# Optimization experiments

Measured on AMD Instinct MI355X. Metric: run time of the kernel, lower is better.

The kernel has to match this reference:

```python
import jax, jax.numpy as jnp
import numpy as np

B, HH, WW, C = 16, 56, 56, 384
HEADS, WS, SHIFT, HID = 12, 7, 3, 1536
N = WS * WS
EPS = 1e-5


def _rel_pos_index(ws):
    coords = np.stack(np.meshgrid(np.arange(ws), np.arange(ws), indexing='ij'))  # (2, ws, ws)
    cf = coords.reshape(2, -1)
    rel = (cf[:, :, None] - cf[:, None, :]).transpose(1, 2, 0).copy()  # (N, N, 2)
    rel[:, :, 0] += ws - 1
    rel[:, :, 1] += ws - 1
    rel[:, :, 0] *= 2 * ws - 1
    return rel.sum(-1)  # (N, N) int


def _attn_mask(H, W, ws, shift):
    img = np.zeros((H, W))
    sl = (slice(0, -ws), slice(-ws, -shift), slice(-shift, None))
    cnt = 0
    for h in sl:
        for w in sl:
            img[h, w] = cnt
            cnt += 1
    mw = img.reshape(H // ws, ws, W // ws, ws).transpose(0, 2, 1, 3).reshape(-1, ws * ws)  # (nW, N)
    am = mw[:, None, :] - mw[:, :, None]
    return np.where(am != 0, -100.0, 0.0).astype(np.float32)  # (nW, N, N)

REL_IDX = jnp.asarray(_rel_pos_index(WS))
ATTN_MASK = jnp.asarray(_attn_mask(HH, WW, WS, SHIFT))


def _ln(x, w, b):
    m = x.mean(-1, keepdims=True)
    v = ((x - m) ** 2).mean(-1, keepdims=True)
    return (x - m) * jax.lax.rsqrt(v + EPS) * w + b


def _win_part(x, ws):
    b, h, w, c = x.shape
    x = x.reshape(b, h // ws, ws, w // ws, ws, c).transpose(0, 1, 3, 2, 4, 5)
    return x.reshape(-1, ws * ws, c)


def _win_rev(wins, ws, h, w):
    c = wins.shape[-1]
    b = wins.shape[0] // ((h // ws) * (w // ws))
    x = wins.reshape(b, h // ws, w // ws, ws, ws, c).transpose(0, 1, 3, 2, 4, 5)
    return x.reshape(b, h, w, c)


def setup_inputs() -> dict:
    key = jax.random.key(0)
    ks = jax.random.split(key, 12)
    s = lambda fan: 1.0 / np.sqrt(fan)
    return {
        'x': jax.random.normal(ks[0], (B, HH * WW, C), jnp.float32),
        'norm1_w': jnp.ones((C,), jnp.float32),
        'norm1_b': jnp.zeros((C,), jnp.float32),
        'qkv_w': jax.random.normal(ks[1], (3 * C, C), jnp.float32) * s(C),
        'qkv_b': jnp.zeros((3 * C,), jnp.float32),
        'bias_table': jax.random.normal(ks[2], ((2 * WS - 1) ** 2, HEADS), jnp.float32) * 0.02,
        'proj_w': jax.random.normal(ks[3], (C, C), jnp.float32) * s(C),
        'proj_b': jnp.zeros((C,), jnp.float32),
        'norm2_w': jnp.ones((C,), jnp.float32),
        'norm2_b': jnp.zeros((C,), jnp.float32),
        'mlp_w1': jax.random.normal(ks[4], (HID, C), jnp.float32) * s(C),
        'mlp_b1': jnp.zeros((HID,), jnp.float32),
        'mlp_w2': jax.random.normal(ks[5], (C, HID), jnp.float32) * s(HID),
        'mlp_b2': jnp.zeros((C,), jnp.float32),
        'H': HH,
        'W': WW,
    }


def reference(x, norm1_w, norm1_b, qkv_w, qkv_b, bias_table, proj_w, proj_b,
              norm2_w, norm2_b, mlp_w1, mlp_b1, mlp_w2, mlp_b2, H, W):
    b = x.shape[0]
    shortcut = x
    h = _ln(x, norm1_w, norm1_b).reshape(b, H, W, C)
    # cyclic shift (H, W divisible by WS -> no padding needed)
    h = jnp.roll(h, shift=(-SHIFT, -SHIFT), axis=(1, 2))
    xw = _win_part(h, WS)  # (b*nW, N, C)
    Bw = xw.shape[0]
    hd = C // HEADS
    qkv = xw @ qkv_w.T + qkv_b  # (Bw, N, 3C)
    qkv = qkv.reshape(Bw, N, 3, HEADS, hd).transpose(2, 0, 3, 1, 4)
    q, k, v = qkv[0], qkv[1], qkv[2]  # (Bw, heads, N, hd)
    attn = jnp.einsum('bhnd,bhmd->bhnm', q * (hd ** -0.5), k)
    rel_bias = bias_table[REL_IDX.reshape(-1)].reshape(N, N, HEADS).transpose(2, 0, 1)
    attn = attn + rel_bias[None]
    nW = ATTN_MASK.shape[0]
    attn = attn.reshape(Bw // nW, nW, HEADS, N, N) + ATTN_MASK[None, :, None]
    attn = jax.nn.softmax(attn.reshape(Bw, HEADS, N, N), axis=-1)
    out = jnp.einsum('bhnm,bhmd->bhnd', attn, v).transpose(0, 2, 1, 3).reshape(Bw, N, C)
    out = out @ proj_w.T + proj_b
    h = _win_rev(out, WS, H, W)
    h = jnp.roll(h, shift=(SHIFT, SHIFT), axis=(1, 2)).reshape(b, H * W, C)
    x = shortcut + h
    y = _ln(x, norm2_w, norm2_b)
    y = jax.nn.gelu(y @ mlp_w1.T + mlp_b1, approximate=False) @ mlp_w2.T + mlp_b2
    return x + y
```

## Files before the change

### kernel.cpp

```cpp
#include <hip/hip_runtime.h>

typedef unsigned short ushort_t;
typedef __attribute__((ext_vector_type(8))) short bf16x8;
typedef __attribute__((ext_vector_type(4))) float f32x4;

__device__ __forceinline__ float b2f(ushort_t u) {
    union { float f; unsigned int u32; } x; x.u32 = ((unsigned int)u) << 16; return x.f;
}
__device__ __forceinline__ ushort_t f2b(float f) {
    union { float f; unsigned int u; } x; x.f = f;
    unsigned int r = x.u + 0x7fffu + ((x.u >> 16) & 1u);
    return (ushort_t)(r >> 16);
}
__device__ __forceinline__ float ldin(const void* p, size_t i, int fp32) {
    return fp32 ? ((const float*)p)[i] : b2f(((const ushort_t*)p)[i]);
}
__device__ __forceinline__ void gl_lds16(const ushort_t* g, ushort_t* l) {
    __builtin_amdgcn_global_load_lds((const __attribute__((address_space(1))) unsigned int*)g,
                                     (__attribute__((address_space(3))) unsigned int*)l, 16, 0, 0);
}
__device__ __forceinline__ float gelu_f(float x) {
    float xx = x * x;
    float u  = x * (0.7978845608028654f + 0.0356774081363f * xx);
    float a  = __builtin_fabsf(u);
    float e2 = __expf(-2.0f * a);
    float t  = (1.0f - e2) * __builtin_amdgcn_rcpf(1.0f + e2);
    t = __builtin_copysignf(t, u);
    return 0.5f * x * (1.0f + t);
}

struct Cv { const void* s; ushort_t* d; int n; };
struct CvA { Cv a[13]; };
__global__ void convert_all(CvA c, int total) {
    int fp32 = (*(const unsigned int*)c.a[0].s == 0x3F800000u);
    for (int idx = blockIdx.x * blockDim.x + threadIdx.x; idx < total; idx += gridDim.x * blockDim.x) {
        int i = idx, k = 0;
        while (k < 12 && i >= c.a[k].n) { i -= c.a[k].n; ++k; }
        c.a[k].d[i] = fp32 ? f2b(((const float*)c.a[k].s)[i]) : ((const ushort_t*)c.a[k].s)[i];
    }
}

__global__ __launch_bounds__(256) void ln_kernel(const void* __restrict__ x,
                                                 const ushort_t* __restrict__ w,
                                                 const ushort_t* __restrict__ bvec,
                                                 ushort_t* __restrict__ out, int mode, int row_base,
                                                 const void* __restrict__ flagsrc)
{
    int wave = threadIdx.x >> 6, lane = threadIdx.x & 63;
    int lr = blockIdx.x * 4 + wave;
    int r = row_base + lr;
    int f32 = (mode == 1) ? 1 : (*(const unsigned int*)flagsrc == 0x3F800000u);
    long src;
    if (mode == 0) {
        int win = r / 49, pos = r % 49;
        int b = win >> 6, wy = (win >> 3) & 7, wx = win & 7;
        int py = pos / 7, px = pos - py * 7;
        int ys = wy * 7 + py + 3; if (ys >= 56) ys -= 56;
        int xs = wx * 7 + px + 3; if (xs >= 56) xs -= 56;
        src = (long)b * 3136 + ys * 56 + xs;
    } else {
        src = r;
    }
    float v[6];
    float s = 0.f, sq = 0.f;
#pragma unroll
    for (int j = 0; j < 6; ++j) {
        v[j] = ldin(x, src * 384 + lane + 64 * j, f32);
        s += v[j]; sq += v[j] * v[j];
    }
#pragma unroll
    for (int off = 32; off; off >>= 1) { s += __shfl_xor(s, off); sq += __shfl_xor(sq, off); }
    float mean = s * (1.f / 384.f);
    float var  = sq * (1.f / 384.f) - mean * mean;
    float rstd = rsqrtf(var + 1e-5f);
    ushort_t* op = out + (size_t)lr * 384;
#pragma unroll
    for (int j = 0; j < 6; ++j) {
        int c = lane + 64 * j;
        op[c] = f2b((v[j] - mean) * rstd * b2f(w[c]) + b2f(bvec[c]));
    }
}

__global__ __launch_bounds__(256) void attn_mfma(const ushort_t* __restrict__ qkv,
                                                 const ushort_t* __restrict__ bt,
                                                 ushort_t* __restrict__ out)
{
    __shared__ __align__(16) ushort_t Pb[4][64 * 72];
    __shared__ __align__(16) ushort_t Vb[4][32 * 72];
    int win = blockIdx.x;
    int t = threadIdx.x;
    int wave = t >> 6, lane = t & 63;
    int quad = lane >> 4, l16 = lane & 15;
    ushort_t* P  = Pb[wave];
    ushort_t* VT = Vb[wave];
    int wimg = win & 63;
    int wy = wimg >> 3, wx = wimg & 7;
    const float scale = 0.17677669529663687f;

    int rjv[4], cjv[4], gjv[4], cvalid[4];
#pragma unroll
    for (int jt = 0; jt < 4; ++jt) {
        int c = jt * 16 + l16;
        cvalid[jt] = (c < 49);
        int rj = c / 7, cj = c - rj * 7;
        rjv[jt] = rj; cjv[jt] = cj;
        int gjy = (wy == 7) ? (rj < 4 ? 1 : 2) : 0;
        int gjx = (wx == 7) ? (cj < 4 ? 1 : 2) : 0;
        gjv[jt] = gjy * 3 + gjx;
    }

    for (int hh = 0; hh < 3; ++hh) {
        int head = wave * 3 + hh;
        size_t base = (size_t)win * 49 * 1152 + (size_t)head * 32;

        bf16x8 qf[4], kf[4];
#pragma unroll
        for (int i = 0; i < 4; ++i) {
            int row = i * 16 + l16;
            bf16x8 z = {};
            qf[i] = z; kf[i] = z;
            if (row < 49) {
                qf[i] = *(const bf16x8*)(qkv + base + (size_t)row * 1152 + quad * 8);
                kf[i] = *(const bf16x8*)(qkv + base + (size_t)row * 1152 + 384 + quad * 8);
            }
        }
#pragma unroll
        for (int e = 0; e < 4; ++e) {
            int j = e * 16 + (lane >> 2);
            int db = (lane & 3) * 8;
            ushort_t buf[8] = {};
            if (j < 49) *(uint4*)buf = *(const uint4*)(qkv + base + (size_t)j * 1152 + 768 + db);
#pragma unroll
            for (int s = 0; s < 8; ++s) VT[(db + s) * 72 + j] = buf[s];
        }

        f32x4 Sv[4][4];
#pragma unroll
        for (int i = 0; i < 4; ++i)
#pragma unroll
            for (int j = 0; j < 4; ++j) {
                f32x4 z = {};
                Sv[i][j] = __builtin_amdgcn_mfma_f32_16x16x32_bf16(qf[i], kf[j], z, 0, 0, 0);
            }

#pragma unroll
        for (int it = 0; it < 4; ++it) {
#pragma unroll
            for (int r = 0; r < 4; ++r) {
                int m = it * 16 + quad * 4 + r;
                int ri = m / 7, ci = m - ri * 7;
                int giy = (wy == 7) ? (ri < 4 ? 1 : 2) : 0;
                int gix = (wx == 7) ? (ci < 4 ? 1 : 2) : 0;
                int gi = giy * 3 + gix;
                float vals[4];
                float vmax = -1e30f;
#pragma unroll
                for (int jt = 0; jt < 4; ++jt) {
                    float sv = -1e30f;
                    if (m < 49 && cvalid[jt]) {
                        int rel = (ri - rjv[jt] + 6) * 13 + (ci - cjv[jt] + 6);
                        sv = Sv[it][jt][r] * scale + b2f(bt[rel * 12 + head]);
                        if (gi != gjv[jt]) sv -= 100.f;
                    }
                    vals[jt] = sv;
                    vmax = fmaxf(vmax, sv);
                }
#pragma unroll
                for (int off = 1; off < 16; off <<= 1) vmax = fmaxf(vmax, __shfl_xor(vmax, off));
                float ssum = 0.f;
#pragma unroll
                for (int jt = 0; jt < 4; ++jt) { float e = __expf(vals[jt] - vmax); vals[jt] = e; ssum += e; }
#pragma unroll
                for (int off = 1; off < 16; off <<= 1) ssum += __shfl_xor(ssum, off);
                float inv = __builtin_amdgcn_rcpf(ssum);
#pragma unroll
                for (int jt = 0; jt < 4; ++jt) P[m * 72 + jt * 16 + l16] = f2b(vals[jt] * inv);
            }
        }

        f32x4 Ov[4][2] = {};
#pragma unroll
        for (int kk = 0; kk < 2; ++kk) {
            bf16x8 vb[2];
            vb[0] = *(const bf16x8*)&VT[(l16) * 72 + kk * 32 + quad * 8];
            vb[1] = *(const bf16x8*)&VT[(16 + l16) * 72 + kk * 32 + quad * 8];
#pragma unroll
            for (int mt = 0; mt < 4; ++mt) {
                bf16x8 pa = *(const bf16x8*)&P[(mt * 16 + l16) * 72 + kk * 32 + quad * 8];
                Ov[mt][0] = __builtin_amdgcn_mfma_f32_16x16x32_bf16(pa, vb[0], Ov[mt][0], 0, 0, 0);
                Ov[mt][1] = __builtin_amdgcn_mfma_f32_16x16x32_bf16(pa, vb[1], Ov[mt][1], 0, 0, 0);
            }
        }
#pragma unroll
        for (int mt = 0; mt < 4; ++mt)
#pragma unroll
            for (int r = 0; r < 4; ++r) {
                int m = mt * 16 + quad * 4 + r;
                if (m < 49) {
                    size_t orow = ((size_t)win * 49 + m) * 384 + (size_t)head * 32;
                    out[orow + l16]      = f2b(Ov[mt][0][r]);
                    out[orow + 16 + l16] = f2b(Ov[mt][1][r]);
                }
            }
    }
}

template <int EPI>
__global__ __launch_bounds__(256) void gemm_k(const ushort_t* __restrict__ A,
                                              const ushort_t* __restrict__ Bw,
                                              const ushort_t* __restrict__ bias,
                                              const void* __restrict__ residv,
                                              void* __restrict__ outv,
                                              int N, int K, long rbase,
                                              const void* __restrict__ flagsrc)
{
    __shared__ __align__(16) ushort_t lA[3][128 * 32];
    __shared__ __align__(16) ushort_t lB[3][128 * 32];

    unsigned gx = gridDim.x;
    unsigned nwg = gx * gridDim.y;
    unsigned lid = blockIdx.y * gx + blockIdx.x;
    unsigned xcd = lid & 7u, chunk_i = lid >> 3;
    unsigned q = nwg >> 3, r8 = nwg & 7u;
    unsigned logical = (xcd < r8 ? xcd * (q + 1) : r8 * (q + 1) + (xcd - r8) * q) + chunk_i;
    int m0 = (int)(logical / gx) * 128, n0 = (int)(logical % gx) * 128;

    int t = threadIdx.x;
    int wave = t >> 6, lane = t & 63;
    int quad = lane >> 4, l16 = lane & 15;
    int wrow = (wave >> 1) * 64, wcol = (wave & 1) * 64;
    f32x4 acc[4][4] = {};

    float bb[4];
#pragma unroll
    for (int j = 0; j < 4; ++j) bb[j] = b2f(bias[n0 + wcol + j * 16 + l16]);
    asm volatile("" :: "v"(bb[0]), "v"(bb[1]), "v"(bb[2]), "v"(bb[3]));

    int srow = wave * 32 + (lane >> 2);
    int fsw  = (srow >> 1) & 3;
    int scol = (((lane & 3) ^ fsw)) * 8;
    const ushort_t* gA0 = A  + (size_t)(m0 + srow) * K + scol;
    const ushort_t* gA1 = gA0 + (size_t)16 * K;
    const ushort_t* gB0 = Bw + (size_t)(n0 + srow) * K + scol;
    const ushort_t* gB1 = gB0 + (size_t)16 * K;

    auto stage = [&](int buf, int k0) {
        gl_lds16(gA0 + k0, &lA[buf][wave * 1024]);
        gl_lds16(gA1 + k0, &lA[buf][wave * 1024 + 512]);
        gl_lds16(gB0 + k0, &lB[buf][wave * 1024]);
        gl_lds16(gB1 + k0, &lB[buf][wave * 1024 + 512]);
    };

    int sl = (quad ^ ((l16 >> 1) & 3)) * 8;
    auto compute = [&](int buf) {
        bf16x8 af[4], bf[4];
#pragma unroll
        for (int i = 0; i < 4; ++i)
            af[i] = *(const bf16x8*)(&lA[buf][(wrow + i * 16 + l16) * 32 + sl]);
#pragma unroll
        for (int j = 0; j < 4; ++j)
            bf[j] = *(const bf16x8*)(&lB[buf][(wcol + j * 16 + l16) * 32 + sl]);
#pragma unroll
        for (int i = 0; i < 4; ++i)
#pragma unroll
            for (int j = 0; j < 4; ++j)
                acc[i][j] = __builtin_amdgcn_mfma_f32_16x16x32_bf16(af[i], bf[j], acc[i][j], 0, 0, 0);
    };

    int T = K >> 5;
    stage(0, 0);
    if (T > 1) stage(1, 32);

    int cur = 0;
    for (int tt = 0; tt < T - 1; ++tt) {
        asm volatile("s_waitcnt vmcnt(4)" ::: "memory");
        __builtin_amdgcn_s_barrier();
        if (tt + 2 < T) stage(cur == 0 ? 2 : cur - 1, (tt + 2) * 32);
        compute(cur);
        cur = (cur == 2) ? 0 : cur + 1;
    }
    asm volatile("s_waitcnt vmcnt(0)" ::: "memory");
    __builtin_amdgcn_s_barrier();
    compute(cur);

    int rf32 = (EPI == 2) ? (*(const unsigned int*)flagsrc == 0x3F800000u) : 1;

#pragma unroll
    for (int i = 0; i < 4; ++i) {
#pragma unroll
        for (int rix = 0; rix < 4; ++rix) {
            int m = m0 + wrow + i * 16 + quad * 4 + rix;
            unsigned orow = 0;
            if (EPI == 2) {
                int mg = (int)rbase + m;
                int win = mg / 49, pos = mg - win * 49;
                int b = win >> 6, wy = (win >> 3) & 7, wx = win & 7;
                int py = pos / 7, px = pos - py * 7;
                int y = wy * 7 + py + 3; if (y >= 56) y -= 56;
                int x = wx * 7 + px + 3; if (x >= 56) x -= 56;
                orow = (unsigned)(b * 3136 + y * 56 + x);
            } else if (EPI == 3) {
                orow = (unsigned)(rbase + m);
            }
#pragma unroll
            for (int j = 0; j < 4; ++j) {
                int n = n0 + wcol + j * 16 + l16;
                float vv = acc[i][j][rix] + bb[j];
                if (EPI == 0) {
                    ((ushort_t*)outv)[(unsigned)m * (unsigned)N + (unsigned)n] = f2b(vv);
                } else if (EPI == 1) {
                    ((ushort_t*)outv)[(unsigned)m * (unsigned)N + (unsigned)n] = f2b(gelu_f(vv));
                } else {
                    float r = ldin(residv, (size_t)orow * 384 + n, rf32);
                    ((float*)outv)[(size_t)orow * 384 + n] = vv + r;
                }
            }
        }
    }
}

extern "C" void kernel_launch(void* const* d_in, const int* in_sizes, int n_in,
                              void* d_out, int out_size, void* d_ws, size_t ws_size,
                              hipStream_t stream)
{
    (void)in_sizes; (void)n_in; (void)out_size;
    char* ws = (char*)d_ws;
    size_t off = 0;
    auto alloc = [&](size_t bytes) { size_t p = off; off = (off + bytes + 255) & ~(size_t)255; return p; };

    size_t o_n1w  = alloc(384 * 2);
    size_t o_n1b  = alloc(384 * 2);
    size_t o_qw   = alloc(442368ull * 2);
    size_t o_qb   = alloc(1152 * 2);
    size_t o_bt   = alloc(2028 * 2);
    size_t o_pw   = alloc(147456ull * 2);
    size_t o_pb   = alloc(384 * 2);
    size_t o_n2w  = alloc(384 * 2);
    size_t o_n2b  = alloc(384 * 2);
    size_t o_w1   = alloc(589824ull * 2);
    size_t o_b1   = alloc(1536 * 2);
    size_t o_w2   = alloc(589824ull * 2);
    size_t o_b2   = alloc(384 * 2);

    size_t avail = (ws_size > off) ? ws_size - off : 0;
    int M_c;
    if      (avail >= (size_t)50176 * 3840 + 1024) M_c = 50176;
    else if (avail >= (size_t)12544 * 3840 + 1024) M_c = 12544;
    else                                            M_c = 6272;
    int nch = 50176 / M_c;
    size_t o_s1 = alloc((size_t)M_c * 768);
    size_t o_s2 = alloc((size_t)M_c * 3072);

    ushort_t* n1w  = (ushort_t*)(ws + o_n1w);
    ushort_t* n1b  = (ushort_t*)(ws + o_n1b);
    ushort_t* qw   = (ushort_t*)(ws + o_qw);
    ushort_t* qb   = (ushort_t*)(ws + o_qb);
    ushort_t* bt   = (ushort_t*)(ws + o_bt);
    ushort_t* pw   = (ushort_t*)(ws + o_pw);
    ushort_t* pb   = (ushort_t*)(ws + o_pb);
    ushort_t* n2w  = (ushort_t*)(ws + o_n2w);
    ushort_t* n2b  = (ushort_t*)(ws + o_n2b);
    ushort_t* w1   = (ushort_t*)(ws + o_w1);
    ushort_t* b1   = (ushort_t*)(ws + o_b1);
    ushort_t* w2   = (ushort_t*)(ws + o_w2);
    ushort_t* b2v  = (ushort_t*)(ws + o_b2);
    ushort_t* s1   = (ushort_t*)(ws + o_s1);
    ushort_t* s2   = (ushort_t*)(ws + o_s2);
    const void* x  = d_in[0];
    const void* fs = d_in[1];
    float* xmid    = (float*)d_out;

    CvA ca;
    ca.a[0]  = {d_in[1],  n1w, 384};
    ca.a[1]  = {d_in[2],  n1b, 384};
    ca.a[2]  = {d_in[3],  qw,  442368};
    ca.a[3]  = {d_in[4],  qb,  1152};
    ca.a[4]  = {d_in[5],  bt,  2028};
    ca.a[5]  = {d_in[6],  pw,  147456};
    ca.a[6]  = {d_in[7],  pb,  384};
    ca.a[7]  = {d_in[8],  n2w, 384};
    ca.a[8]  = {d_in[9],  n2b, 384};
    ca.a[9]  = {d_in[10], w1,  589824};
    ca.a[10] = {d_in[11], b1,  1536};
    ca.a[11] = {d_in[12], w2,  589824};
    ca.a[12] = {d_in[13], b2v, 384};
    convert_all<<<2048, 256, 0, stream>>>(ca, 1776492);

    for (int c = 0; c < nch; ++c) {
        int rb = c * M_c;
        ln_kernel<<<dim3(M_c / 4), dim3(256), 0, stream>>>(x, n1w, n1b, s1, 0, rb, fs);
        gemm_k<0><<<dim3(9, M_c / 128), dim3(256), 0, stream>>>(s1, qw, qb, nullptr, s2, 1152, 384, 0, fs);
        attn_mfma<<<dim3(M_c / 49), dim3(256), 0, stream>>>(s2, bt, s1);
        gemm_k<2><<<dim3(3, M_c / 128), dim3(256), 0, stream>>>(s1, pw, pb, x, xmid, 384, 384, rb, fs);
    }
    for (int c = 0; c < nch; ++c) {
        int rb = c * M_c;
        ln_kernel<<<dim3(M_c / 4), dim3(256), 0, stream>>>(xmid, n2w, n2b, s1, 1, rb, fs);
        gemm_k<1><<<dim3(12, M_c / 128), dim3(256), 0, stream>>>(s1, w1, b1, nullptr, s2, 1536, 384, 0, fs);
        gemm_k<3><<<dim3(3, M_c / 128), dim3(256), 0, stream>>>(s2, w2, b2v, xmid, (float*)d_out, 384, 1536, rb, fs);
    }
}
```

Before: 623.8 us.

## Enlarge GEMM tile to 256x128 with 8 waves per block

Changes the GEMM kernel from 128x128 tiles with 4 waves to 256x128 tiles with 8 waves. Each block now stages 256 A rows and 128 B rows per k-step using three async global-to-LDS loads per wave, with M clamping and bounds checks for a partial last tile. The intent is to reuse each B tile across more rows and cut per-block overhead. In exchange, each block uses more LDS, the grid has fewer blocks (which can hurt occupancy and wave balance), and the prefetch wait count is adjusted.

```diff
diff --git a/kernel.cpp b/kernel.cpp
--- a/kernel.cpp
+++ b/kernel.cpp
@@ -206,15 +206,15 @@
 }
 
 template <int EPI>
-__global__ __launch_bounds__(256) void gemm_k(const ushort_t* __restrict__ A,
-                                              const ushort_t* __restrict__ Bw,
-                                              const ushort_t* __restrict__ bias,
-                                              const void* __restrict__ residv,
-                                              void* __restrict__ outv,
-                                              int N, int K, long rbase,
-                                              const void* __restrict__ flagsrc)
+__global__ __launch_bounds__(512, 4) void gemm_k(const ushort_t* __restrict__ A,
+                                                 const ushort_t* __restrict__ Bw,
+                                                 const ushort_t* __restrict__ bias,
+                                                 const void* __restrict__ residv,
+                                                 void* __restrict__ outv,
+                                                 int N, int K, int Mp, long rbase,
+                                                 const void* __restrict__ flagsrc)
 {
-    __shared__ __align__(16) ushort_t lA[3][128 * 32];
+    __shared__ __align__(16) ushort_t lA[3][256 * 32];
     __shared__ __align__(16) ushort_t lB[3][128 * 32];
 
     unsigned gx = gridDim.x;
@@ -223,7 +223,7 @@
     unsigned xcd = lid & 7u, chunk_i = lid >> 3;
     unsigned q = nwg >> 3, r8 = nwg & 7u;
     unsigned logical = (xcd < r8 ? xcd * (q + 1) : r8 * (q + 1) + (xcd - r8) * q) + chunk_i;
-    int m0 = (int)(logical / gx) * 128, n0 = (int)(logical % gx) * 128;
+    int m0 = (int)(logical / gx) * 256, n0 = (int)(logical % gx) * 128;
 
     int t = threadIdx.x;
     int wave = t >> 6, lane = t & 63;
@@ -236,19 +236,27 @@
     for (int j = 0; j < 4; ++j) bb[j] = b2f(bias[n0 + wcol + j * 16 + l16]);
     asm volatile("" :: "v"(bb[0]), "v"(bb[1]), "v"(bb[2]), "v"(bb[3]));
 
-    int srow = wave * 32 + (lane >> 2);
-    int fsw  = (srow >> 1) & 3;
-    int scol = (((lane & 3) ^ fsw)) * 8;
-    const ushort_t* gA0 = A  + (size_t)(m0 + srow) * K + scol;
-    const ushort_t* gA1 = gA0 + (size_t)16 * K;
-    const ushort_t* gB0 = Bw + (size_t)(n0 + srow) * K + scol;
-    const ushort_t* gB1 = gB0 + (size_t)16 * K;
+    const ushort_t* gp[3];
+    ushort_t* lp[3];
+    int lstr[3];
+#pragma unroll
+    for (int e = 0; e < 3; ++e) {
+        int chunk = wave * 3 + e;
+        int a = (chunk < 16);
+        int trow = (a ? chunk * 16 : (chunk - 16) * 16) + (lane >> 2);
+        int fsw = (trow >> 1) & 3;
+        int scol = ((lane & 3) ^ fsw) * 8;
+        int grow = a ? (m0 + trow) : (n0 + trow);
+        if (a && grow >= Mp) grow = Mp - 1;
+        gp[e] = (a ? A : Bw) + (size_t)grow * K + scol;
+        lp[e] = a ? &lA[0][chunk * 512] : &lB[0][(chunk - 16) * 512];
+        lstr[e] = a ? 256 * 32 : 128 * 32;
+    }
 
     auto stage = [&](int buf, int k0) {
-        gl_lds16(gA0 + k0, &lA[buf][wave * 1024]);
-        gl_lds16(gA1 + k0, &lA[buf][wave * 1024 + 512]);
-        gl_lds16(gB0 + k0, &lB[buf][wave * 1024]);
-        gl_lds16(gB1 + k0, &lB[buf][wave * 1024 + 512]);
+#pragma unroll
+        for (int e = 0; e < 3; ++e)
+            gl_lds16(gp[e] + k0, lp[e] + buf * lstr[e]);
     };
 
     int sl = (quad ^ ((l16 >> 1) & 3)) * 8;
@@ -269,11 +277,11 @@
 
     int T = K >> 5;
     stage(0, 0);
-    if (T > 1) stage(1, 32);
+    stage(1, 32);
 
     int cur = 0;
     for (int tt = 0; tt < T - 1; ++tt) {
-        asm volatile("s_waitcnt vmcnt(4)" ::: "memory");
+        asm volatile("s_waitcnt vmcnt(3)" ::: "memory");
         __builtin_amdgcn_s_barrier();
         if (tt + 2 < T) stage(cur == 0 ? 2 : cur - 1, (tt + 2) * 32);
         compute(cur);
@@ -290,6 +298,7 @@
 #pragma unroll
         for (int rix = 0; rix < 4; ++rix) {
             int m = m0 + wrow + i * 16 + quad * 4 + rix;
+            if (m >= Mp) continue;
             unsigned orow = 0;
             if (EPI == 2) {
                 int mg = (int)rbase + m;
@@ -388,15 +397,17 @@
 
     for (int c = 0; c < nch; ++c) {
         int rb = c * M_c;
+        int gy = (M_c + 255) / 256;
         ln_kernel<<<dim3(M_c / 4), dim3(256), 0, stream>>>(x, n1w, n1b, s1, 0, rb, fs);
-        gemm_k<0><<<dim3(9, M_c / 128), dim3(256), 0, stream>>>(s1, qw, qb, nullptr, s2, 1152, 384, 0, fs);
+        gemm_k<0><<<dim3(9, gy), dim3(512), 0, stream>>>(s1, qw, qb, nullptr, s2, 1152, 384, M_c, 0, fs);
         attn_mfma<<<dim3(M_c / 49), dim3(256), 0, stream>>>(s2, bt, s1);
-        gemm_k<2><<<dim3(3, M_c / 128), dim3(256), 0, stream>>>(s1, pw, pb, x, xmid, 384, 384, rb, fs);
+        gemm_k<2><<<dim3(3, gy), dim3(512), 0, stream>>>(s1, pw, pb, x, xmid, 384, 384, M_c, rb, fs);
     }
     for (int c = 0; c < nch; ++c) {
         int rb = c * M_c;
+        int gy = (M_c + 255) / 256;
         ln_kernel<<<dim3(M_c / 4), dim3(256), 0, stream>>>(xmid, n2w, n2b, s1, 1, rb, fs);
-        gemm_k<1><<<dim3(12, M_c / 128), dim3(256), 0, stream>>>(s1, w1, b1, nullptr, s2, 1536, 384, 0, fs);
-        gemm_k<3><<<dim3(3, M_c / 128), dim3(256), 0, stream>>>(s2, w2, b2v, xmid, (float*)d_out, 384, 1536, rb, fs);
-    }
-}
+        gemm_k<1><<<dim3(12, gy), dim3(512), 0, stream>>>(s1, w1, b1, nullptr, s2, 1536, 384, M_c, 0, fs);
+        gemm_k<3><<<dim3(3, gy), dim3(512), 0, stream>>>(s2, w2, b2v, xmid, (float*)d_out, 384, 1536, M_c, rb, fs);
+    }
+}
```

After: 594.0 us. 1.05x faster.

## Load GEMM A fragments directly to registers, stage only B through LDS

Applied to the files above, without the earlier changes.

The GEMM kernel no longer stages the A tile through shared memory. Each wave loads its A MFMA fragments straight from global memory into registers, double-buffered across k-steps, while B keeps the triple-buffered LDS pipeline. This halves LDS use so launch bounds can request three blocks per CU, and MFMA sections are wrapped in setprio. The trade-off is uncoalesced, partly redundant global reads of A, since each wave pair reads the same rows, plus higher register pressure.

```diff
diff --git a/kernel.cpp b/kernel.cpp
--- a/kernel.cpp
+++ b/kernel.cpp
@@ -206,15 +206,14 @@
 }
 
 template <int EPI>
-__global__ __launch_bounds__(256) void gemm_k(const ushort_t* __restrict__ A,
-                                              const ushort_t* __restrict__ Bw,
-                                              const ushort_t* __restrict__ bias,
-                                              const void* __restrict__ residv,
-                                              void* __restrict__ outv,
-                                              int N, int K, long rbase,
-                                              const void* __restrict__ flagsrc)
+__global__ __launch_bounds__(256, 3) void gemm_k(const ushort_t* __restrict__ A,
+                                                 const ushort_t* __restrict__ Bw,
+                                                 const ushort_t* __restrict__ bias,
+                                                 const void* __restrict__ residv,
+                                                 void* __restrict__ outv,
+                                                 int N, int K, long rbase,
+                                                 const void* __restrict__ flagsrc)
 {
-    __shared__ __align__(16) ushort_t lA[3][128 * 32];
     __shared__ __align__(16) ushort_t lB[3][128 * 32];
 
     unsigned gx = gridDim.x;
@@ -231,58 +230,70 @@
     int wrow = (wave >> 1) * 64, wcol = (wave & 1) * 64;
     f32x4 acc[4][4] = {};
 
-    float bb[4];
-#pragma unroll
-    for (int j = 0; j < 4; ++j) bb[j] = b2f(bias[n0 + wcol + j * 16 + l16]);
-    asm volatile("" :: "v"(bb[0]), "v"(bb[1]), "v"(bb[2]), "v"(bb[3]));
-
-    int srow = wave * 32 + (lane >> 2);
-    int fsw  = (srow >> 1) & 3;
-    int scol = (((lane & 3) ^ fsw)) * 8;
-    const ushort_t* gA0 = A  + (size_t)(m0 + srow) * K + scol;
-    const ushort_t* gA1 = gA0 + (size_t)16 * K;
-    const ushort_t* gB0 = Bw + (size_t)(n0 + srow) * K + scol;
-    const ushort_t* gB1 = gB0 + (size_t)16 * K;
-
-    auto stage = [&](int buf, int k0) {
-        gl_lds16(gA0 + k0, &lA[buf][wave * 1024]);
-        gl_lds16(gA1 + k0, &lA[buf][wave * 1024 + 512]);
-        gl_lds16(gB0 + k0, &lB[buf][wave * 1024]);
-        gl_lds16(gB1 + k0, &lB[buf][wave * 1024 + 512]);
+    int srow0 = wave * 16 + (lane >> 2);
+    int srow1 = srow0 + 64;
+    int sc0 = ((lane & 3) ^ ((srow0 >> 1) & 3)) * 8;
+    int sc1 = ((lane & 3) ^ ((srow1 >> 1) & 3)) * 8;
+    const ushort_t* gB0 = Bw + (size_t)(n0 + srow0) * K + sc0;
+    const ushort_t* gB1 = Bw + (size_t)(n0 + srow1) * K + sc1;
+    ushort_t* lBp = &lB[0][0];
+    auto stage = [&](int bufbase, int k0) {
+        gl_lds16(gB0 + k0, lBp + bufbase + wave * 512);
+        gl_lds16(gB1 + k0, lBp + bufbase + (wave + 4) * 512);
     };
 
+    const ushort_t* gA[4];
+#pragma unroll
+    for (int i = 0; i < 4; ++i)
+        gA[i] = A + (size_t)(m0 + wrow + i * 16 + l16) * K + quad * 8;
+    auto loadA = [&](bf16x8 (&d)[4], int k0) {
+#pragma unroll
+        for (int i = 0; i < 4; ++i) d[i] = *(const bf16x8*)(gA[i] + k0);
+    };
+
     int sl = (quad ^ ((l16 >> 1) & 3)) * 8;
-    auto compute = [&](int buf) {
-        bf16x8 af[4], bf[4];
-#pragma unroll
-        for (int i = 0; i < 4; ++i)
-            af[i] = *(const bf16x8*)(&lA[buf][(wrow + i * 16 + l16) * 32 + sl]);
+    auto compute = [&](int bufbase, const bf16x8 (&af)[4]) {
+        bf16x8 bf[4];
 #pragma unroll
         for (int j = 0; j < 4; ++j)
-            bf[j] = *(const bf16x8*)(&lB[buf][(wcol + j * 16 + l16) * 32 + sl]);
+            bf[j] = *(const bf16x8*)(lBp + bufbase + (wcol + j * 16 + l16) * 32 + sl);
+        __builtin_amdgcn_s_setprio(1);
 #pragma unroll
         for (int i = 0; i < 4; ++i)
 #pragma unroll
             for (int j = 0; j < 4; ++j)
                 acc[i][j] = __builtin_amdgcn_mfma_f32_16x16x32_bf16(af[i], bf[j], acc[i][j], 0, 0, 0);
+        __builtin_amdgcn_s_setprio(0);
     };
 
     int T = K >> 5;
+    bf16x8 aA[4], aB[4];
+    loadA(aA, 0);
     stage(0, 0);
-    if (T > 1) stage(1, 32);
-
-    int cur = 0;
-    for (int tt = 0; tt < T - 1; ++tt) {
-        asm volatile("s_waitcnt vmcnt(4)" ::: "memory");
+    stage(4096, 32);
+
+    int cb = 0, ss = 2;
+    for (int tt = 0; tt < T; tt += 2) {
+        if (tt < T - 1) asm volatile("s_waitcnt vmcnt(2)" ::: "memory");
+        else            asm volatile("s_waitcnt vmcnt(0)" ::: "memory");
         __builtin_amdgcn_s_barrier();
-        if (tt + 2 < T) stage(cur == 0 ? 2 : cur - 1, (tt + 2) * 32);
-        compute(cur);
-        cur = (cur == 2) ? 0 : cur + 1;
-    }
-    asm volatile("s_waitcnt vmcnt(0)" ::: "memory");
-    __builtin_amdgcn_s_barrier();
-    compute(cur);
-
+        if (tt + 1 < T) loadA(aB, (tt + 1) * 32);
+        if (tt + 2 < T) { stage(ss * 4096, (tt + 2) * 32); ss = (ss == 2) ? 0 : ss + 1; }
+        compute(cb * 4096, aA);
+        cb = (cb == 2) ? 0 : cb + 1;
+        int t1 = tt + 1;
+        if (t1 < T - 1) asm volatile("s_waitcnt vmcnt(2)" ::: "memory");
+        else            asm volatile("s_waitcnt vmcnt(0)" ::: "memory");
+        __builtin_amdgcn_s_barrier();
+        if (t1 + 1 < T) loadA(aA, (t1 + 1) * 32);
+        if (t1 + 2 < T) { stage(ss * 4096, (t1 + 2) * 32); ss = (ss == 2) ? 0 : ss + 1; }
+        compute(cb * 4096, aB);
+        cb = (cb == 2) ? 0 : cb + 1;
+    }
+
+    float bb[4];
+#pragma unroll
+    for (int j = 0; j < 4; ++j) bb[j] = b2f(bias[n0 + wcol + j * 16 + l16]);
     int rf32 = (EPI == 2) ? (*(const unsigned int*)flagsrc == 0x3F800000u) : 1;
 
 #pragma unroll
@@ -388,15 +399,17 @@
 
     for (int c = 0; c < nch; ++c) {
         int rb = c * M_c;
+        int gy = M_c / 128;
         ln_kernel<<<dim3(M_c / 4), dim3(256), 0, stream>>>(x, n1w, n1b, s1, 0, rb, fs);
-        gemm_k<0><<<dim3(9, M_c / 128), dim3(256), 0, stream>>>(s1, qw, qb, nullptr, s2, 1152, 384, 0, fs);
+        gemm_k<0><<<dim3(9, gy), dim3(256), 0, stream>>>(s1, qw, qb, nullptr, s2, 1152, 384, 0, fs);
         attn_mfma<<<dim3(M_c / 49), dim3(256), 0, stream>>>(s2, bt, s1);
-        gemm_k<2><<<dim3(3, M_c / 128), dim3(256), 0, stream>>>(s1, pw, pb, x, xmid, 384, 384, rb, fs);
+        gemm_k<2><<<dim3(3, gy), dim3(256), 0, stream>>>(s1, pw, pb, x, xmid, 384, 384, rb, fs);
     }
     for (int c = 0; c < nch; ++c) {
         int rb = c * M_c;
+        int gy = M_c / 128;
         ln_kernel<<<dim3(M_c / 4), dim3(256), 0, stream>>>(xmid, n2w, n2b, s1, 1, rb, fs);
-        gemm_k<1><<<dim3(12, M_c / 128), dim3(256), 0, stream>>>(s1, w1, b1, nullptr, s2, 1536, 384, 0, fs);
-        gemm_k<3><<<dim3(3, M_c / 128), dim3(256), 0, stream>>>(s2, w2, b2v, xmid, (float*)d_out, 384, 1536, rb, fs);
-    }
-}
+        gemm_k<1><<<dim3(12, gy), dim3(256), 0, stream>>>(s1, w1, b1, nullptr, s2, 1536, 384, 0, fs);
+        gemm_k<3><<<dim3(3, gy), dim3(256), 0, stream>>>(s2, w2, b2v, xmid, (float*)d_out, 384, 1536, rb, fs);
+    }
+}
```

After: 754.9 us. 1.21x slower.
